# Kernel tuning notes

Hardware: AMD Instinct MI355X
Metric: run time of the kernel (lower is better)

## Reference

```python
import jax, jax.numpy as jnp
import numpy as np

GROUPS = 32
EPS = 1e-6


def group_norm(x, gamma, beta):
    b, c, h, w = x.shape
    xg = x.reshape(b, GROUPS, c // GROUPS, h, w)
    mean = xg.mean(axis=(2, 3, 4), keepdims=True)
    var = xg.var(axis=(2, 3, 4), keepdims=True)
    xn = (xg - mean) * jax.lax.rsqrt(var + EPS)
    xn = xn.reshape(b, c, h, w)
    return xn * gamma[None, :, None, None] + beta[None, :, None, None]


def conv1x1(x, w, b):
    # x: [B,C,H,W], w: [O,C], b: [O]
    return jnp.einsum('bchw,oc->bohw', x, w) + b[None, :, None, None]


def setup_inputs() -> dict:
    key = jax.random.key(0)
    ks = jax.random.split(key, 6)
    C = 512
    B, H, W = 2, 64, 64
    s = (C) ** -0.5  # fan-in style init scale for 1x1 convs
    return {
        'x': jax.random.normal(ks[0], (B, C, H, W), jnp.float32),
        'gn_gamma': jnp.ones((C,), jnp.float32),
        'gn_beta': jnp.zeros((C,), jnp.float32),
        'wq': jax.random.normal(ks[1], (C, C), jnp.float32) * s,
        'bq': jnp.zeros((C,), jnp.float32),
        'wk': jax.random.normal(ks[2], (C, C), jnp.float32) * s,
        'bk': jnp.zeros((C,), jnp.float32),
        'wv': jax.random.normal(ks[3], (C, C), jnp.float32) * s,
        'bv': jnp.zeros((C,), jnp.float32),
        'wo': jax.random.normal(ks[4], (C, C), jnp.float32) * s,
        'bo': jnp.zeros((C,), jnp.float32),
    }


def reference(x, gn_gamma, gn_beta, wq, bq, wk, bk, wv, bv, wo, bo):
    b, c, h, w = x.shape
    n = h * w
    h_ = group_norm(x, gn_gamma, gn_beta)
    q = conv1x1(h_, wq, bq).reshape(b, c, n)   # [B,C,N]
    k = conv1x1(h_, wk, bk).reshape(b, c, n)   # [B,C,N]
    v = conv1x1(h_, wv, bv).reshape(b, c, n)   # [B,C,N]
    scale = jnp.asarray(int(c) ** (-0.5), x.dtype)
    # scores[b, nq, nk] = sum_c q[b,c,nq] * k[b,c,nk]
    scores = jnp.einsum('bcn,bcm->bnm', q, k) * scale
    attn = jax.nn.softmax(scores, axis=2)      # softmax over keys
    # out[b,c,nq] = sum_m v[b,c,m] * attn[b,nq,m]
    out = jnp.einsum('bcm,bnm->bcn', v, attn).reshape(b, c, h, w)
    out = conv1x1(out, wo, bo)
    return x + out
```

## Files before the change

### kernel.cpp

```cpp
#include <hip/hip_runtime.h>

typedef unsigned short u16;
typedef __attribute__((ext_vector_type(8))) unsigned short ushort8;
typedef __attribute__((ext_vector_type(8))) short bf16x8;
typedef __attribute__((ext_vector_type(4))) float f32x4;

#define DEVINL __device__ __forceinline__

DEVINL float bf2f(u16 u){ union{unsigned i; float f;} v; v.i = ((unsigned)u) << 16; return v.f; }
DEVINL u16 f2bf(float f){
  unsigned x = __builtin_bit_cast(unsigned, f);
  x += 0x7fffu + ((x >> 16) & 1u);
  return (u16)(x >> 16);
}
DEVINL void gl_lds16(const void* g, void* l){
  __builtin_amdgcn_global_load_lds((const __attribute__((address_space(1))) unsigned*)g,
                                   (__attribute__((address_space(3))) unsigned*)l, 16, 0, 0);
}
template<int N> DEVINL void wait_vmcnt(){
  asm volatile("s_waitcnt vmcnt(%0)" :: "n"(N) : "memory");
}
DEVINL void hard_barrier(){
  asm volatile("" ::: "memory");
  __builtin_amdgcn_s_barrier();
  asm volatile("" ::: "memory");
}
DEVINL float wsum(float v){
  #pragma unroll
  for (int o = 32; o; o >>= 1) v += __shfl_xor(v, o, 64);
  return v;
}

__global__ __launch_bounds__(256) void cvt4b_k(const float* __restrict__ s0, const float* __restrict__ s1,
                 const float* __restrict__ s2, const float* __restrict__ s3,
                 const float* __restrict__ bq, const float* __restrict__ bk, const float* __restrict__ bv,
                 u16* __restrict__ wdst, float* __restrict__ bdst){
  if (blockIdx.x == 512){
    for (int j = threadIdx.x; j < 1536; j += 256)
      bdst[j] = (j < 512) ? bq[j] : (j < 1024) ? bk[j-512] : bv[j-1024];
    return;
  }
  const int g = blockIdx.x >> 7;
  const float* src = (g==0) ? s0 : (g==1) ? s1 : (g==2) ? s2 : s3;
  const int i = ((blockIdx.x & 127)*256 + threadIdx.x)*8;
  float4 f0 = *(const float4*)(src + i);
  float4 f1 = *(const float4*)(src + i + 4);
  ushort8 o;
  o[0]=f2bf(f0.x); o[1]=f2bf(f0.y); o[2]=f2bf(f0.z); o[3]=f2bf(f0.w);
  o[4]=f2bf(f1.x); o[5]=f2bf(f1.y); o[6]=f2bf(f1.z); o[7]=f2bf(f1.w);
  *(ushort8*)(wdst + g*262144 + i) = o;
}

__global__ __launch_bounds__(256) void reduce4_k(const u16* __restrict__ part,
                 const float* __restrict__ psum, u16* __restrict__ dst){
  __shared__ float invsh[4];
  const int t = threadIdx.x, w = t>>6, ln = t&63;
  const int row = blockIdx.x*4 + w;
  float s = psum[ln*8192 + blockIdx.y*4096 + row];
  s = wsum(s);
  if (ln == 0) invsh[w] = 1.f / s;
  __syncthreads();
  const int i = (blockIdx.x*256 + t)*8;
  const u16* p = part + (size_t)blockIdx.y*8388608;
  float a[8] = {};
  #pragma unroll
  for (int ks = 0; ks < 4; ++ks){
    ushort8 u = *(const ushort8*)(p + (size_t)ks*2097152 + i);
    #pragma unroll
    for (int j = 0; j < 8; ++j) a[j] += bf2f(u[j]);
  }
  const float iv = invsh[w];
  ushort8 o;
  #pragma unroll
  for (int j = 0; j < 8; ++j) o[j] = f2bf(a[j] * iv);
  *(ushort8*)(dst + (size_t)blockIdx.y*2097152 + i) = o;
}

__global__ __launch_bounds__(256) void gn_stats_k(const float* __restrict__ x, float* __restrict__ stats){
  __shared__ __align__(16) float red[8];
  const float* px = x + ((size_t)blockIdx.x << 16);
  const int t = threadIdx.x;
  float s = 0.f, ss = 0.f;
  for (int off = t*4; off < 65536; off += 1024){
    float4 u = *(const float4*)(px + off);
    s  += u.x + u.y + u.z + u.w;
    ss += u.x*u.x + u.y*u.y + u.z*u.z + u.w*u.w;
  }
  s = wsum(s); ss = wsum(ss);
  if ((t & 63) == 0){ red[t>>6] = s; red[4+(t>>6)] = ss; }
  __syncthreads();
  if (t == 0){
    float S1 = red[0]+red[1]+red[2]+red[3];
    float S2 = red[4]+red[5]+red[6]+red[7];
    float mean = S1 * (1.f/65536.f);
    float var  = S2 * (1.f/65536.f) - mean*mean;
    stats[2*blockIdx.x]   = mean;
    stats[2*blockIdx.x+1] = rsqrtf(var + 1e-6f);
  }
}

__global__ __launch_bounds__(256) void gn_apply_k(const float* __restrict__ x, const float* __restrict__ gamma,
                 const float* __restrict__ beta, const float* __restrict__ stats, u16* __restrict__ ht){
  __shared__ __align__(16) u16 tile[32*512];
  const int b = blockIdx.y, n0 = blockIdx.x*32, t = threadIdx.x;
  #pragma unroll
  for (int it = 0; it < 8; ++it){
    int c  = it*64 + (t>>2);
    int nn = (t&3)*8;
    const float* px = x + ((size_t)(b*512 + c) << 12) + n0 + nn;
    float4 u0 = *(const float4*)(px);
    float4 u1 = *(const float4*)(px + 4);
    float mean = stats[2*(b*32 + (c>>4))];
    float rstd = stats[2*(b*32 + (c>>4)) + 1];
    float ga = gamma[c], be = beta[c];
    float f[8] = {u0.x,u0.y,u0.z,u0.w,u1.x,u1.y,u1.z,u1.w};
    #pragma unroll
    for (int j = 0; j < 8; ++j)
      tile[(nn+j)*512 + c] = f2bf((f[j] - mean) * rstd * ga + be);
  }
  __syncthreads();
  const int rw = t>>3, sg = t&7;
  #pragma unroll
  for (int uu = 0; uu < 8; ++uu){
    ushort8 v = *(const ushort8*)(tile + rw*512 + sg*64 + uu*8);
    *(ushort8*)(ht + ((size_t)(b*4096 + n0 + rw) << 9) + sg*64 + uu*8) = v;
  }
}

template<bool EXPSUM>
__global__ __launch_bounds__(512) void gemm8_nt(
    const u16* __restrict__ A, const u16* __restrict__ Bt, u16* __restrict__ C,
    float* __restrict__ psum,
    int K, int lda, int ldb, int ldc, int zdiv,
    long long aStrB, long long aStr, long long bStrB, long long bStr,
    long long cStrB, long long cStr)
{
  extern __shared__ __align__(16) char smem[];
  const int z = blockIdx.z, z1 = z / zdiv, z2 = z % zdiv;
  A  += (size_t)aStrB*z1 + (size_t)aStr*z2;
  Bt += (size_t)bStrB*z1 + (size_t)bStr*z2;
  C  += (size_t)cStrB*z1 + (size_t)cStr*z2;
  const int nwg = gridDim.x*gridDim.y;
  int wg = blockIdx.y*gridDim.x + blockIdx.x;
  wg = (wg & 7)*(nwg >> 3) + (wg >> 3);
  const int m0 = (wg / gridDim.x)*256, n0 = (wg % gridDim.x)*256;

  const int t = threadIdx.x, wv = t>>6, ln = t&63;
  const int wm = wv>>2, wn = wv&3;
  const int lq = ln&15, lg = ln>>4;
  const int srow = ln>>2;
  const int sseg = (((ln&3) ^ ((srow>>1)&3)))*8;
  const int rslot = (lg ^ ((lq>>1)&3))*16;

  auto STAGE_A = [&](int u){
    char* base = smem + (u&1)*16384 + wv*1024;
    const u16* g = A + (size_t)(m0 + wv*16 + srow)*lda + u*32 + sseg;
    gl_lds16(g, base);
    gl_lds16(g + (size_t)128*lda, base + 8192);
  };
  auto STAGE_B = [&](int u){
    char* base = smem + 32768 + (u&1)*16384 + wv*1024;
    const u16* g = Bt + (size_t)(n0 + wv*16 + srow)*ldb + u*32 + sseg;
    gl_lds16(g, base);
    gl_lds16(g + (size_t)128*ldb, base + 8192);
  };
  auto LDA4 = [&](int u, int mh, bf16x8* a){
    const char* p = smem + (u&1)*16384 + (wm*128 + mh*64 + lq)*64 + rslot;
    #pragma unroll
    for (int i = 0; i < 4; ++i) a[i] = *(const bf16x8*)(p + i*1024);
  };
  auto LDB4 = [&](int u, bf16x8* b){
    const char* p = smem + 32768 + (u&1)*16384 + (wn*64 + lq)*64 + rslot;
    #pragma unroll
    for (int j = 0; j < 4; ++j) b[j] = *(const bf16x8*)(p + j*1024);
  };

  f32x4 acc[8][4] = {};
  auto MFMA16 = [&](bf16x8* a4, bf16x8* b4, int moff){
    __builtin_amdgcn_s_setprio(1);
    #pragma unroll
    for (int n = 0; n < 4; ++n)
      #pragma unroll
      for (int m = 0; m < 4; ++m)
        acc[moff+m][n] = __builtin_amdgcn_mfma_f32_16x16x32_bf16(a4[m], b4[n], acc[moff+m][n], 0, 0, 0);
    __builtin_amdgcn_s_setprio(0);
  };

  STAGE_A(0); STAGE_B(0);
  const int U = K >> 5;
  for (int u = 0; u < U; ++u){
    wait_vmcnt<0>();
    hard_barrier();
    bf16x8 a0[4], a1[4], b[4];
    LDA4(u, 0, a0); LDB4(u, b);
    if (u + 1 < U){ STAGE_A(u+1); STAGE_B(u+1); }
    MFMA16(a0, b, 0);
    LDA4(u, 1, a1);
    MFMA16(a1, b, 4);
  }
  const int slice = EXPSUM ? ((n0 >> 8)*4 + wn) : 0;
  #pragma unroll
  for (int m = 0; m < 8; ++m)
    #pragma unroll
    for (int r2 = 0; r2 < 4; ++r2){
      const int mg = m0 + wm*128 + m*16 + lg*4 + r2;
      u16* cp = C + (size_t)mg*ldc + n0 + wn*64 + lq;
      if constexpr (EXPSUM){
        float e[4], rs = 0.f;
        #pragma unroll
        for (int n = 0; n < 4; ++n){ e[n] = __expf(acc[m][n][r2]); rs += e[n]; }
        rs += __shfl_xor(rs, 1, 64);
        rs += __shfl_xor(rs, 2, 64);
        rs += __shfl_xor(rs, 4, 64);
        rs += __shfl_xor(rs, 8, 64);
        if (lq == 0) psum[slice*8192 + z1*4096 + mg] = rs;
        #pragma unroll
        for (int n = 0; n < 4; ++n) cp[n*16] = f2bf(e[n]);
      } else {
        #pragma unroll
        for (int n = 0; n < 4; ++n) cp[n*16] = f2bf(acc[m][n][r2]);
      }
    }
}

__global__ __launch_bounds__(256) void qkv_k(
    const u16* __restrict__ Wstk, const u16* __restrict__ ht,
    const float* __restrict__ biases, u16* __restrict__ dstBase)
{
  __shared__ __align__(16) char smem[32768];
  char* smA0 = smem;
  char* smA1 = smem + 8192;
  char* smB0 = smem + 16384;
  char* smB1 = smem + 24576;
  const int z = blockIdx.z, mat = z >> 1, b = z & 1;
  const u16* A  = Wstk + mat*262144;
  const u16* Bt = ht + (size_t)b*2097152;
  const float* bias = biases + mat*512;
  const float oscale = (mat == 0) ? 0.044194173824159216f : 1.0f;
  u16* dst = dstBase + (size_t)mat*4194304 + (size_t)b*2097152;
  const int m0 = blockIdx.y*128, n0 = blockIdx.x*128;
  const int t = threadIdx.x, wv = t>>6, ln = t&63;
  const int wm = wv>>1, wn = wv&1;
  const int lq = ln&15, lg = ln>>4;
  const int srow = ln>>2;
  const int sseg = (((ln&3) ^ ((srow>>1)&3)))*8;
  const int rslot = (lg ^ ((lq>>1)&3))*16;
  f32x4 acc[4][4] = {};
  for (int kk = 0; kk < 512; kk += 64){
    __syncthreads();
    #pragma unroll
    for (int r = 0; r < 2; ++r){
      const int rr = r*64 + wv*16;
      const u16* pa = A  + (size_t)(m0 + rr + srow)*512 + kk + sseg;
      const u16* pb = Bt + (size_t)(n0 + rr + srow)*512 + kk + sseg;
      gl_lds16(pa,      smA0 + rr*64);
      gl_lds16(pa + 32, smA1 + rr*64);
      gl_lds16(pb,      smB0 + rr*64);
      gl_lds16(pb + 32, smB1 + rr*64);
    }
    __syncthreads();
    #pragma unroll
    for (int half = 0; half < 2; ++half){
      const char* pA = half ? smA1 : smA0;
      const char* pB = half ? smB1 : smB0;
      bf16x8 af[4], bfv[4];
      #pragma unroll
      for (int i = 0; i < 4; ++i) af[i]  = *(const bf16x8*)(pA + ((wm*64 + i*16 + lq)<<6) + rslot);
      #pragma unroll
      for (int j = 0; j < 4; ++j) bfv[j] = *(const bf16x8*)(pB + ((wn*64 + j*16 + lq)<<6) + rslot);
      #pragma unroll
      for (int i = 0; i < 4; ++i)
        #pragma unroll
        for (int j = 0; j < 4; ++j)
          acc[i][j] = __builtin_amdgcn_mfma_f32_16x16x32_bf16(af[i], bfv[j], acc[i][j], 0, 0, 0);
    }
  }
  if (mat == 2){
    #pragma unroll
    for (int i = 0; i < 4; ++i)
      #pragma unroll
      for (int r2 = 0; r2 < 4; ++r2){
        const int mg = m0 + wm*64 + i*16 + lg*4 + r2;
        float bv = bias[mg];
        #pragma unroll
        for (int j = 0; j < 4; ++j){
          const int ng = n0 + wn*64 + j*16 + lq;
          dst[(size_t)mg*4096 + ng] = f2bf(acc[i][j][r2] + bv);
        }
      }
  } else {
    __syncthreads();
    u16* ct = (u16*)smem;
    #pragma unroll
    for (int i = 0; i < 4; ++i)
      #pragma unroll
      for (int j = 0; j < 4; ++j)
        #pragma unroll
        for (int r2 = 0; r2 < 4; ++r2){
          const int ml = wm*64 + i*16 + lg*4 + r2;
          const int nl = wn*64 + j*16 + lq;
          ct[nl*128 + ml] = f2bf((acc[i][j][r2] + bias[m0 + ml]) * oscale);
        }
    __syncthreads();
    const int rw = t>>1, hf = (t&1)*64;
    #pragma unroll
    for (int u = 0; u < 8; ++u){
      *(ushort8*)(dst + (size_t)(n0 + rw)*512 + m0 + hf + u*8) =
          *(const ushort8*)(ct + rw*128 + hf + u*8);
    }
  }
}

template<bool TRANS_OUT, bool HAS_BIAS, bool HAS_RES, bool F32OUT>
__global__ __launch_bounds__(256) void gemm_nt(
    const u16* __restrict__ A, const u16* __restrict__ Bt,
    const float* __restrict__ bias, const float* __restrict__ res, void* __restrict__ Cw_,
    int K, int lda, int ldb, int ldc, int zdiv,
    long long aStrB, long long aStr, long long bStrB, long long bStr,
    long long cStrB, long long cStr, long long rStrB, float oscale)
{
  __shared__ __align__(16) char smem[32768];
  char* smA0 = smem;
  char* smA1 = smem + 8192;
  char* smB0 = smem + 16384;
  char* smB1 = smem + 24576;
  const int z = blockIdx.z;
  const int z1 = z / zdiv, z2 = z % zdiv;
  A  += (size_t)aStrB*z1 + (size_t)aStr*z2;
  Bt += (size_t)bStrB*z1 + (size_t)bStr*z2;
  u16*   Cw16 = (u16*)Cw_   + (size_t)cStrB*z1 + (size_t)cStr*z2;
  float* Cw32 = (float*)Cw_ + (size_t)cStrB*z1 + (size_t)cStr*z2;
  const float* resp = HAS_RES ? (res + (size_t)rStrB*z1) : nullptr;
  const int m0 = blockIdx.y*128, n0 = blockIdx.x*128;
  const int t = threadIdx.x, wv = t>>6, ln = t&63;
  const int wm = wv>>1, wn = wv&1;
  const int lq = ln&15, lg = ln>>4;
  const int srow = ln>>2;
  const int sseg = (((ln&3) ^ ((srow>>1)&3)))*8;
  const int rslot = (lg ^ ((lq>>1)&3))*16;
  f32x4 acc[4][4] = {};
  for (int kk = 0; kk < K; kk += 64){
    __syncthreads();
    #pragma unroll
    for (int r = 0; r < 2; ++r){
      const int rr = r*64 + wv*16;
      const u16* pa = A  + (size_t)(m0 + rr + srow)*lda + kk + sseg;
      const u16* pb = Bt + (size_t)(n0 + rr + srow)*ldb + kk + sseg;
      gl_lds16(pa,      smA0 + rr*64);
      gl_lds16(pa + 32, smA1 + rr*64);
      gl_lds16(pb,      smB0 + rr*64);
      gl_lds16(pb + 32, smB1 + rr*64);
    }
    __syncthreads();
    #pragma unroll
    for (int half = 0; half < 2; ++half){
      const char* pA = half ? smA1 : smA0;
      const char* pB = half ? smB1 : smB0;
      bf16x8 af[4], bfv[4];
      #pragma unroll
      for (int i = 0; i < 4; ++i) af[i]  = *(const bf16x8*)(pA + ((wm*64 + i*16 + lq)<<6) + rslot);
      #pragma unroll
      for (int j = 0; j < 4; ++j) bfv[j] = *(const bf16x8*)(pB + ((wn*64 + j*16 + lq)<<6) + rslot);
      #pragma unroll
      for (int i = 0; i < 4; ++i)
        #pragma unroll
        for (int j = 0; j < 4; ++j)
          acc[i][j] = __builtin_amdgcn_mfma_f32_16x16x32_bf16(af[i], bfv[j], acc[i][j], 0, 0, 0);
    }
  }
  if constexpr (!TRANS_OUT){
    #pragma unroll
    for (int i = 0; i < 4; ++i){
      #pragma unroll
      for (int r2 = 0; r2 < 4; ++r2){
        const int mg = m0 + wm*64 + i*16 + lg*4 + r2;
        float bv = HAS_BIAS ? bias[mg] : 0.f;
        #pragma unroll
        for (int j = 0; j < 4; ++j){
          const int ng = n0 + wn*64 + j*16 + lq;
          float v = (acc[i][j][r2] + bv) * oscale;
          if (HAS_RES) v += resp[(size_t)mg*ldc + ng];
          if constexpr (F32OUT) Cw32[(size_t)mg*ldc + ng] = v;
          else                  Cw16[(size_t)mg*ldc + ng] = f2bf(v);
        }
      }
    }
  } else {
    __syncthreads();
    u16* ct = (u16*)smem;
    #pragma unroll
    for (int i = 0; i < 4; ++i)
      #pragma unroll
      for (int j = 0; j < 4; ++j)
        #pragma unroll
        for (int r2 = 0; r2 < 4; ++r2){
          const int ml = wm*64 + i*16 + lg*4 + r2;
          const int nl = wn*64 + j*16 + lq;
          float v = acc[i][j][r2];
          if (HAS_BIAS) v += bias[m0 + ml];
          ct[nl*128 + ml] = f2bf(v * oscale);
        }
    __syncthreads();
    const int rw = t>>1, hf = (t&1)*64;
    #pragma unroll
    for (int u = 0; u < 8; ++u){
      *(ushort8*)(Cw16 + (size_t)(n0 + rw)*ldc + m0 + hf + u*8) =
          *(const ushort8*)(ct + rw*128 + hf + u*8);
    }
  }
}

extern "C" void kernel_launch(void* const* d_in, const int* in_sizes, int n_in,
                              void* d_out, int out_size, void* d_ws, size_t ws_size,
                              hipStream_t stream)
{
  const float* x   = (const float*)d_in[0];
  const float* gam = (const float*)d_in[1];
  const float* bet = (const float*)d_in[2];
  const float* wq  = (const float*)d_in[3];
  const float* bq  = (const float*)d_in[4];
  const float* wk  = (const float*)d_in[5];
  const float* bk  = (const float*)d_in[6];
  const float* wvp = (const float*)d_in[7];
  const float* bv  = (const float*)d_in[8];
  const float* wo  = (const float*)d_in[9];
  const float* bo  = (const float*)d_in[10];
  float* out = (float*)d_out;

  char* w = (char*)d_ws;
  float* stats   = (float*)w;
  float* psum    = (float*)(w + 4096);
  float* biasQKV = (float*)(w + 2134016);
  u16* wqb  = (u16*)(w + (size_t)4194304);
  u16* wob  = wqb + 3*262144;
  u16* Qt   = wqb + 4*262144;
  u16* Kt   = Qt + 4194304;
  u16* Vb   = Kt + 4194304;
  u16* attT = Vb + 4194304;
  u16* Sbuf = attT + 4194304;
  u16* part = Sbuf + 33554432;
  u16* ht   = (u16*)d_out;

  const long long NC = 4096LL*512, NN = 4096LL*4096;

  cvt4b_k<<<dim3(513), dim3(256), 0, stream>>>(wq, wk, wvp, wo, bq, bk, bv, wqb, biasQKV);
  gn_stats_k<<<dim3(64), dim3(256), 0, stream>>>(x, stats);
  gn_apply_k<<<dim3(128,2), dim3(256), 0, stream>>>(x, gam, bet, stats, ht);
  qkv_k<<<dim3(32,4,6), dim3(256), 0, stream>>>(wqb, ht, biasQKV, Qt);
  gemm8_nt<true><<<dim3(16,16,2), dim3(512), 65536, stream>>>(
      Qt, Kt, Sbuf, psum, 512, 512, 512, 4096, 1, NC, 0, NC, 0, NN, 0);
  gemm8_nt<false><<<dim3(2,16,8), dim3(512), 65536, stream>>>(
      Sbuf, Vb, part, nullptr, 1024, 4096, 4096, 512, 4,
      NN, 1024, NC, 1024, 8388608, 2097152);
  reduce4_k<<<dim3(1024,2), dim3(256), 0, stream>>>(part, psum, attT);
  gemm_nt<false, true, true, true><<<dim3(32,4,2), dim3(256), 0, stream>>>(
      wob, attT, bo, x, out, 512, 512, 512, 4096, 1, 0,0, NC,0, NC,0, NC, 1.0f);
}
```

Before: 184.0 us.

## Deepen gemm8_nt LDS pipeline to four stages with register double-buffering

```diff
diff --git a/kernel.cpp b/kernel.cpp
--- a/kernel.cpp
+++ b/kernel.cpp
@@ -153,50 +153,57 @@
   const int rslot = (lg ^ ((lq>>1)&3))*16;
 
   auto STAGE_A = [&](int u){
-    char* base = smem + (u&1)*16384 + wv*1024;
+    char* base = smem + (u&3)*16384 + wv*1024;
     const u16* g = A + (size_t)(m0 + wv*16 + srow)*lda + u*32 + sseg;
     gl_lds16(g, base);
     gl_lds16(g + (size_t)128*lda, base + 8192);
   };
   auto STAGE_B = [&](int u){
-    char* base = smem + 32768 + (u&1)*16384 + wv*1024;
+    char* base = smem + 65536 + (u&3)*16384 + wv*1024;
     const u16* g = Bt + (size_t)(n0 + wv*16 + srow)*ldb + u*32 + sseg;
     gl_lds16(g, base);
     gl_lds16(g + (size_t)128*ldb, base + 8192);
   };
-  auto LDA4 = [&](int u, int mh, bf16x8* a){
-    const char* p = smem + (u&1)*16384 + (wm*128 + mh*64 + lq)*64 + rslot;
-    #pragma unroll
-    for (int i = 0; i < 4; ++i) a[i] = *(const bf16x8*)(p + i*1024);
+  auto LDA8 = [&](int u, bf16x8* a){
+    const char* p = smem + (u&3)*16384 + (wm*128 + lq)*64 + rslot;
+    #pragma unroll
+    for (int i = 0; i < 8; ++i) a[i] = *(const bf16x8*)(p + i*1024);
   };
   auto LDB4 = [&](int u, bf16x8* b){
-    const char* p = smem + 32768 + (u&1)*16384 + (wn*64 + lq)*64 + rslot;
+    const char* p = smem + 65536 + (u&3)*16384 + (wn*64 + lq)*64 + rslot;
     #pragma unroll
     for (int j = 0; j < 4; ++j) b[j] = *(const bf16x8*)(p + j*1024);
   };
 
   f32x4 acc[8][4] = {};
-  auto MFMA16 = [&](bf16x8* a4, bf16x8* b4, int moff){
+  auto MFMA32 = [&](bf16x8* a8, bf16x8* b4){
     __builtin_amdgcn_s_setprio(1);
     #pragma unroll
     for (int n = 0; n < 4; ++n)
       #pragma unroll
-      for (int m = 0; m < 4; ++m)
-        acc[moff+m][n] = __builtin_amdgcn_mfma_f32_16x16x32_bf16(a4[m], b4[n], acc[moff+m][n], 0, 0, 0);
+      for (int m = 0; m < 8; ++m)
+        acc[m][n] = __builtin_amdgcn_mfma_f32_16x16x32_bf16(a8[m], b4[n], acc[m][n], 0, 0, 0);
     __builtin_amdgcn_s_setprio(0);
   };
 
-  STAGE_A(0); STAGE_B(0);
+  bf16x8 aC[8], bC[4], aN[8], bN[4];
+  STAGE_A(0); STAGE_B(0); STAGE_A(1); STAGE_B(1); STAGE_A(2); STAGE_B(2);
+  wait_vmcnt<8>();
+  hard_barrier();
+  LDA8(0, aC); LDB4(0, bC);
   const int U = K >> 5;
-  for (int u = 0; u < U; ++u){
-    wait_vmcnt<0>();
+  for (int u = 0; u < U; u += 2){
+    if (u+3 < U){ STAGE_A(u+3); STAGE_B(u+3); }
+    if (u+1 < U){ LDA8(u+1, aN); LDB4(u+1, bN); }
+    MFMA32(aC, bC);
+    if (u+3 < U) wait_vmcnt<8>(); else wait_vmcnt<0>();
     hard_barrier();
-    bf16x8 a0[4], a1[4], b[4];
-    LDA4(u, 0, a0); LDB4(u, b);
-    if (u + 1 < U){ STAGE_A(u+1); STAGE_B(u+1); }
-    MFMA16(a0, b, 0);
-    LDA4(u, 1, a1);
-    MFMA16(a1, b, 4);
+    const int v = u + 1;
+    if (v+3 < U){ STAGE_A(v+3); STAGE_B(v+3); }
+    if (v+1 < U){ LDA8(v+1, aC); LDB4(v+1, bC); }
+    MFMA32(aN, bN);
+    if (v+3 < U) wait_vmcnt<8>(); else wait_vmcnt<0>();
+    hard_barrier();
   }
   const int slice = EXPSUM ? ((n0 >> 8)*4 + wn) : 0;
   #pragma unroll
@@ -447,9 +454,9 @@
   gn_stats_k<<<dim3(64), dim3(256), 0, stream>>>(x, stats);
   gn_apply_k<<<dim3(128,2), dim3(256), 0, stream>>>(x, gam, bet, stats, ht);
   qkv_k<<<dim3(32,4,6), dim3(256), 0, stream>>>(wqb, ht, biasQKV, Qt);
-  gemm8_nt<true><<<dim3(16,16,2), dim3(512), 65536, stream>>>(
+  gemm8_nt<true><<<dim3(16,16,2), dim3(512), 131072, stream>>>(
       Qt, Kt, Sbuf, psum, 512, 512, 512, 4096, 1, NC, 0, NC, 0, NN, 0);
-  gemm8_nt<false><<<dim3(2,16,8), dim3(512), 65536, stream>>>(
+  gemm8_nt<false><<<dim3(2,16,8), dim3(512), 131072, stream>>>(
       Sbuf, Vb, part, nullptr, 1024, 4096, 4096, 512, 4,
       NN, 1024, NC, 1024, 8388608, 2097152);
   reduce4_k<<<dim3(1024,2), dim3(256), 0, stream>>>(part, psum, attT);
```

New measurement: 187.9 us. 1.02x slower.
